# Optimization experiments

Measured on AMD Instinct MI355X. Metric: run time of the kernel, lower is better.

The kernel has to match this reference:

```python
import jax, jax.numpy as jnp
import numpy as np

B = 32            # graphs in batch
NPG = 2048        # nodes per graph (equal-size graphs -> static topk sizes)
N = B * NPG
DEG = 8
E = N * DEG
IN = 64
H1 = 2 * IN       # 128
H2 = 2 * H1       # 256
K1 = NPG // 2     # SAGPooling ratio=0.5
K2 = K1 // 2
EPS = 1e-5


def _lin(k, fi, fo):
    s = 1.0 / np.sqrt(fi)
    return jax.random.uniform(k, (fi, fo), jnp.float32, -s, s)


def setup_inputs() -> dict:
    key = jax.random.key(0)
    ks = jax.random.split(key, 24)
    x = jax.random.normal(ks[0], (N, IN), jnp.float32)
    # edges strictly within each graph
    eg = jnp.repeat(jnp.arange(B, dtype=jnp.int32), NPG * DEG)
    src = eg * NPG + jax.random.randint(ks[1], (E,), 0, NPG, jnp.int32)
    tgt = eg * NPG + jax.random.randint(ks[2], (E,), 0, NPG, jnp.int32)
    edge_index = jnp.stack([src, tgt])
    batch = jnp.repeat(jnp.arange(B, dtype=jnp.int32), NPG)
    return {
        "x": x, "edge_index": edge_index, "batch": batch,
        # SAGEConv1: lin_l (neighbors, with bias) + lin_r (root, no bias)
        "W1l": _lin(ks[3], IN, H1), "b1l": jnp.zeros((H1,), jnp.float32),
        "W1r": _lin(ks[4], IN, H1),
        "bn1_g": jnp.ones((H1,), jnp.float32), "bn1_b": jnp.zeros((H1,), jnp.float32),
        # SAGPooling1 scorer = GraphConv(H1, 1): lin_rel (sum-agg, bias) + lin_root
        "p1_Wrel": _lin(ks[5], H1, 1), "p1_brel": jnp.zeros((1,), jnp.float32),
        "p1_Wroot": _lin(ks[6], H1, 1),
        "W2l": _lin(ks[7], H1, H2), "b2l": jnp.zeros((H2,), jnp.float32),
        "W2r": _lin(ks[8], H1, H2),
        "bn2_g": jnp.ones((H2,), jnp.float32), "bn2_b": jnp.zeros((H2,), jnp.float32),
        "p2_Wrel": _lin(ks[9], H2, 1), "p2_brel": jnp.zeros((1,), jnp.float32),
        "p2_Wroot": _lin(ks[10], H2, 1),
        "Wlin": _lin(ks[11], H2, 2), "blin": jnp.zeros((2,), jnp.float32),
    }


def sage_conv(x, src, tgt, emask, Wl, bl, Wr, n):
    # PyG SAGEConv: mean-aggregate x_j over valid incoming edges, then lin_l(agg)+lin_r(x)
    msg = x[src] * emask[:, None]
    s = jax.ops.segment_sum(msg, tgt, num_segments=n)
    cnt = jax.ops.segment_sum(emask, tgt, num_segments=n)
    mean = s / jnp.maximum(cnt, 1.0)[:, None]
    return mean @ Wl + bl + x @ Wr


def graph_conv_score(x, src, tgt, emask, Wrel, brel, Wroot, n):
    # PyG GraphConv (sum aggregation), out_channels=1
    s = jax.ops.segment_sum(x[src] * emask[:, None], tgt, num_segments=n)
    return (s @ Wrel + brel + x @ Wroot)[:, 0]


def batch_norm(x, g, b):
    m = x.mean(0)
    v = jnp.mean((x - m) ** 2, 0)  # biased var, as BatchNorm1d training
    return (x - m) * jax.lax.rsqrt(v + EPS) * g + b


def sag_pool(x, src, tgt, emask, score, npg, k):
    # per-graph top-k by score; x_kept scaled by tanh(score); edges re-filtered via mask
    vals, idx = jax.lax.top_k(score.reshape(B, npg), k)          # [B,k]
    perm = (jnp.arange(B, dtype=jnp.int32)[:, None] * npg + idx.astype(jnp.int32)).reshape(-1)
    xnew = x[perm] * jnp.tanh(vals.reshape(-1))[:, None]
    mapping = jnp.full((x.shape[0],), -1, jnp.int32).at[perm].set(
        jnp.arange(B * k, dtype=jnp.int32))
    ns, nt = mapping[src], mapping[tgt]
    valid = emask * ((ns >= 0) & (nt >= 0)).astype(emask.dtype)
    return xnew, jnp.maximum(ns, 0), jnp.maximum(nt, 0), valid


def reference(x, edge_index, batch, W1l, b1l, W1r, bn1_g, bn1_b,
              p1_Wrel, p1_brel, p1_Wroot, W2l, b2l, W2r, bn2_g, bn2_b,
              p2_Wrel, p2_brel, p2_Wroot, Wlin, blin):
    src, tgt = edge_index[0], edge_index[1]
    emask = jnp.ones((src.shape[0],), x.dtype)

    h = sage_conv(x, src, tgt, emask, W1l, b1l, W1r, N)
    h = jax.nn.relu(batch_norm(h, bn1_g, bn1_b))
    s1 = graph_conv_score(h, src, tgt, emask, p1_Wrel, p1_brel, p1_Wroot, N)
    h, src, tgt, emask = sag_pool(h, src, tgt, emask, s1, NPG, K1)

    n1 = B * K1
    h = sage_conv(h, src, tgt, emask, W2l, b2l, W2r, n1)
    h = jax.nn.relu(batch_norm(h, bn2_g, bn2_b))
    s2 = graph_conv_score(h, src, tgt, emask, p2_Wrel, p2_brel, p2_Wroot, n1)
    h, src, tgt, emask = sag_pool(h, src, tgt, emask, s2, K1, K2)

    batch2 = jnp.repeat(jnp.arange(B, dtype=jnp.int32), K2)
    pooled = jax.ops.segment_sum(h, batch2, num_segments=B) / jnp.asarray(K2, h.dtype)
    out = jax.nn.relu(pooled) @ Wlin + blin
    return jax.nn.softmax(out, axis=1)
```

## Files before the change

### kernel.cpp

```cpp
#include <hip/hip_runtime.h>
#include <math.h>

#define Bg   32
#define NPGc 2048
#define Nn   (Bg*NPGc)
#define DEGc 8
#define Ee   (Nn*DEGc)
#define INc  64
#define H1c  128
#define H2c  256
#define K1c  1024
#define K2c  512
#define N1c  (Bg*K1c)
#define N2c  (Bg*K2c)
#define SLAB 64

typedef __attribute__((ext_vector_type(8))) short short8;
typedef __attribute__((ext_vector_type(4))) float f32x4;

__device__ __forceinline__ ushort f2bf(float f) {
    uint u = __float_as_uint(f);
    uint r = (u + 0x7fffu + ((u >> 16) & 1u)) >> 16;
    return (ushort)r;
}
__device__ __forceinline__ float bf2f(ushort v) { return __uint_as_float((uint)v << 16); }
__device__ __forceinline__ float bfhi(uint v) { return __uint_as_float(v & 0xffff0000u); }
__device__ __forceinline__ float bflo(uint v) { return __uint_as_float(v << 16); }
__device__ __forceinline__ uint fkey(float f) {
    uint u = __float_as_uint(f);
    return u ^ ((uint)((int)u >> 31) | 0x80000000u);
}
__device__ __forceinline__ void unpk8(uint4 v, float* f) {
    f[0] = bflo(v.x); f[1] = bfhi(v.x);
    f[2] = bflo(v.y); f[3] = bfhi(v.y);
    f[4] = bflo(v.z); f[5] = bfhi(v.z);
    f[6] = bflo(v.w); f[7] = bfhi(v.w);
}
__device__ __forceinline__ uint4 pack8(const float* a, float inv) {
    uint4 o;
    o.x = (uint)f2bf(a[0] * inv) | ((uint)f2bf(a[1] * inv) << 16);
    o.y = (uint)f2bf(a[2] * inv) | ((uint)f2bf(a[3] * inv) << 16);
    o.z = (uint)f2bf(a[4] * inv) | ((uint)f2bf(a[5] * inv) << 16);
    o.w = (uint)f2bf(a[6] * inv) | ((uint)f2bf(a[7] * inv) << 16);
    return o;
}
__device__ __forceinline__ void accf8(float* a, const float* p) {
    float4 u0 = *(const float4*)p;
    float4 u1 = *(const float4*)(p + 4);
    a[0] += u0.x; a[1] += u0.y; a[2] += u0.z; a[3] += u0.w;
    a[4] += u1.x; a[5] += u1.y; a[6] += u1.z; a[7] += u1.w;
}

__global__ void init_kernel(int4* __restrict__ wc1, int4* __restrict__ wc2,
                            int4* __restrict__ dstats) {
    int id = blockIdx.x * blockDim.x + threadIdx.x;
    int4 z = {0, 0, 0, 0};
    if (id < 16384) { wc1[id] = z; return; }
    id -= 16384;
    if (id < 8192)  { wc2[id] = z; return; }
    id -= 8192;
    if (id < 384)   { dstats[id] = z; }
}

__global__ void prep2_kernel(const int* __restrict__ src, const int* __restrict__ tgt,
                             const float* __restrict__ W1l, const float* __restrict__ W1r,
                             const float* __restrict__ W2l, const float* __restrict__ W2r,
                             ushort* __restrict__ T1l, ushort* __restrict__ T1r,
                             ushort* __restrict__ T2l, ushort* __restrict__ T2r,
                             int* __restrict__ wc1, int* __restrict__ col1) {
    int id = blockIdx.x * blockDim.x + threadIdx.x;
    if (id < Ee) {
        int t = tgt[id];
        int p = atomicAdd(&wc1[t], 1);
        col1[t * SLAB + p] = src[id];
        return;
    }
    id -= Ee;
    if (id < 8192) {
        int c = id / 64, k = id % 64;
        T1l[id] = f2bf(W1l[k * 128 + c]);
        T1r[id] = f2bf(W1r[k * 128 + c]);
        return;
    }
    id -= 8192;
    if (id < 32768) {
        int c = id / 128, k = id % 128;
        T2l[id] = f2bf(W2l[k * 256 + c]);
        T2r[id] = f2bf(W2r[k * 256 + c]);
    }
}
#define PREP2_TOTAL (Ee + 8192 + 32768)

__global__ __launch_bounds__(512) void gemm1f_kernel(
        const float* __restrict__ x, const int* __restrict__ deg,
        const int* __restrict__ col, const ushort* __restrict__ Wtl,
        const ushort* __restrict__ Wtr, const float* __restrict__ bias,
        ushort* __restrict__ out, double* __restrict__ dsum,
        double* __restrict__ dsq) {
    __shared__ ushort As[2][128][36];
    __shared__ ushort Bs[2][128][36];
    __shared__ float bsumS[2][128], bsqS[2][128];
    int b = blockIdx.x;
    int bs = ((b & 7) << 6) + (b >> 3);
    int m0 = bs << 7;
    int lane = threadIdx.x & 63;
    int wid = threadIdx.x >> 6;
    int wr = (wid & 1) << 6, wc = (wid >> 1) << 5;
    int l16 = lane & 15, quad = lane >> 4;

    int ar = threadIdx.x >> 2, ack = (threadIdx.x & 3) * 8;
    int anode = m0 + ar;
    int abg = anode * SLAB, adg = deg[anode];
    int4 c0h = *(const int4*)&col[abg];
    int4 c1h = *(const int4*)&col[abg + 4];
    int anb[8] = {c0h.x, c0h.y, c0h.z, c0h.w, c1h.x, c1h.y, c1h.z, c1h.w};

    f32x4 acc[4][2];
#pragma unroll
    for (int a = 0; a < 4; a++)
#pragma unroll
        for (int c = 0; c < 2; c++) acc[a][c] = (f32x4){0.f, 0.f, 0.f, 0.f};

    for (int kk0 = 0; kk0 < INc; kk0 += 32) {
        {
            int idx = threadIdx.x;
            int r = idx >> 2, ck = (idx & 3) * 8;
            *(uint4*)&Bs[0][r][ck] = *(const uint4*)&Wtl[(size_t)r * INc + kk0 + ck];
            *(uint4*)&Bs[1][r][ck] = *(const uint4*)&Wtr[(size_t)r * INc + kk0 + ck];
        }
        {
            const float* xp = &x[(size_t)anode * INc + kk0 + ack];
            float vals[8];
            float4 v0 = *(const float4*)xp, v1 = *(const float4*)(xp + 4);
            vals[0] = v0.x; vals[1] = v0.y; vals[2] = v0.z; vals[3] = v0.w;
            vals[4] = v1.x; vals[5] = v1.y; vals[6] = v1.z; vals[7] = v1.w;
            *(uint4*)&As[1][ar][ack] = pack8(vals, 1.f);
        }
        {
            float a[8] = {0.f, 0.f, 0.f, 0.f, 0.f, 0.f, 0.f, 0.f};
#pragma unroll
            for (int j = 0; j < 8; j++)
                if (j < adg) accf8(a, &x[(size_t)anb[j] * INc + kk0 + ack]);
            for (int i = abg + 8; i < abg + adg; i++)
                accf8(a, &x[(size_t)col[i] * INc + kk0 + ack]);
            int cdg = adg < 1 ? 1 : adg;
            *(uint4*)&As[0][ar][ack] = pack8(a, 1.f / (float)cdg);
        }
        __syncthreads();
        short8 a[2][4], bfr[2][2];
#pragma unroll
        for (int s = 0; s < 2; s++)
#pragma unroll
            for (int mt = 0; mt < 4; mt++)
                a[s][mt] = *(const short8*)&As[s][wr + mt * 16 + l16][quad * 8];
#pragma unroll
        for (int s = 0; s < 2; s++)
#pragma unroll
            for (int nt = 0; nt < 2; nt++)
                bfr[s][nt] = *(const short8*)&Bs[s][wc + nt * 16 + l16][quad * 8];
#pragma unroll
        for (int mt = 0; mt < 4; mt++)
#pragma unroll
            for (int nt = 0; nt < 2; nt++) {
                acc[mt][nt] = __builtin_amdgcn_mfma_f32_16x16x32_bf16(
                    a[0][mt], bfr[0][nt], acc[mt][nt], 0, 0, 0);
                acc[mt][nt] = __builtin_amdgcn_mfma_f32_16x16x32_bf16(
                    a[1][mt], bfr[1][nt], acc[mt][nt], 0, 0, 0);
            }
        __syncthreads();
    }
    float s[2] = {0.f, 0.f}, sq[2] = {0.f, 0.f};
#pragma unroll
    for (int nt = 0; nt < 2; nt++) {
        int colx = wc + nt * 16 + l16;
        float bv = bias[colx];
#pragma unroll
        for (int mt = 0; mt < 4; mt++)
#pragma unroll
            for (int rr = 0; rr < 4; rr++) {
                int row = m0 + wr + mt * 16 + quad * 4 + rr;
                float ov = acc[mt][nt][rr] + bv;
                out[(size_t)row * H1c + colx] = f2bf(ov);
                s[nt] += ov; sq[nt] += ov * ov;
            }
    }
#pragma unroll
    for (int nt = 0; nt < 2; nt++) {
        float ss = s[nt], qq = sq[nt];
        ss += __shfl_down(ss, 16); qq += __shfl_down(qq, 16);
        ss += __shfl_down(ss, 32); qq += __shfl_down(qq, 32);
        if (quad == 0) {
            bsumS[wid & 1][wc + nt * 16 + l16] = ss;
            bsqS[wid & 1][wc + nt * 16 + l16] = qq;
        }
    }
    __syncthreads();
    if (threadIdx.x < 128) {
        int c = threadIdx.x;
        atomicAdd(&dsum[c], (double)(bsumS[0][c] + bsumS[1][c]));
        atomicAdd(&dsq[c], (double)(bsqS[0][c] + bsqS[1][c]));
    }
}

template<int C>
__global__ __launch_bounds__(256) void score_kernel(const ushort* __restrict__ h,
                                                    const double* __restrict__ dsum,
                                                    const double* __restrict__ dsq,
                                                    const float* __restrict__ g,
                                                    const float* __restrict__ b,
                                                    const float* __restrict__ wrel,
                                                    const float* __restrict__ wroot,
                                                    float* __restrict__ r,
                                                    float* __restrict__ root, int n) {
    __shared__ float sc[C], sh[C], wrl[C], wrt[C];
    if ((int)threadIdx.x < C) {
        int c = threadIdx.x;
        double m = dsum[c] / (double)n;
        double var = dsq[c] / (double)n - m * m;
        float s = g[c] * (float)(1.0 / sqrt(var + 1e-5));
        sc[c] = s; sh[c] = b[c] - (float)m * s;
        wrl[c] = wrel[c]; wrt[c] = wroot[c];
    }
    __syncthreads();
    int gid = blockIdx.x * 256 + threadIdx.x;
    int node = gid >> 3, ln = gid & 7;
    float rr = 0.f, rt = 0.f;
#pragma unroll
    for (int p = 0; p < C / 64; p++) {
        int cb = p * 64 + ln * 8;
        uint4 v = *(const uint4*)&h[(size_t)node * C + cb];
        float vv[8];
        unpk8(v, vv);
#pragma unroll
        for (int q = 0; q < 8; q++) {
            int cc = cb + q;
            float val = fmaxf(vv[q] * sc[cc] + sh[cc], 0.f);
            rr += val * wrl[cc];
            rt += val * wrt[cc];
        }
    }
#pragma unroll
    for (int off = 4; off; off >>= 1) {
        rr += __shfl_down(rr, off);
        rt += __shfl_down(rt, off);
    }
    if (ln == 0) { r[node] = rr; root[node] = rt; }
}

__global__ void __launch_bounds__(1024) sel1_kernel(const float* __restrict__ r,
                                                    const float* __restrict__ root,
                                                    const int* __restrict__ deg,
                                                    const int* __restrict__ col,
                                                    const float* __restrict__ brel,
                                                    int* __restrict__ perm,
                                                    float* __restrict__ tval,
                                                    int* __restrict__ map) {
    __shared__ float rL[2048];
    __shared__ float svals[2048];
    __shared__ uint hist[257];
    __shared__ uint wsum[16];
    __shared__ uint s_b, s_rem;
    int g = blockIdx.x;
    int tid = threadIdx.x;
    int lane = tid & 63, wid = tid >> 6;
    int base = g * NPGc;
    rL[tid] = r[base + tid];
    rL[tid + 1024] = r[base + tid + 1024];
    if (tid < 257) hist[tid] = 0;
    __syncthreads();
    float bv = brel[0];
#pragma unroll
    for (int j = 0; j < 2; j++) {
        int i = tid + (j << 10);
        int node = base + i;
        float acc = bv + root[node];
        int e0 = node * SLAB, dg = deg[node];
        int4 c0 = *(const int4*)&col[e0];
        int4 c1 = *(const int4*)&col[e0 + 4];
        int nb[8] = {c0.x, c0.y, c0.z, c0.w, c1.x, c1.y, c1.z, c1.w};
#pragma unroll
        for (int q = 0; q < 8; q++)
            if (q < dg) acc += rL[nb[q] - base];
        for (int e = e0 + 8; e < e0 + dg; e++) acc += rL[col[e] - base];
        svals[i] = acc;
    }
    __syncthreads();

    uint prefix = 0, himask = 0, rem = (uint)K1c;
    for (int shift = 24; shift >= 0; shift -= 8) {
#pragma unroll
        for (int j = 0; j < 2; j++) {
            uint kk = fkey(svals[tid + (j << 10)]);
            if ((kk & himask) == prefix) atomicAdd(&hist[(kk >> shift) & 255], 1);
        }
        __syncthreads();
        if (tid < 64) {
            int L = tid;
            uint h0 = hist[4 * L], h1v = hist[4 * L + 1], h2v = hist[4 * L + 2],
                 h3 = hist[4 * L + 3];
            uint s3 = h3, s2 = h2v + s3, s1 = h1v + s2, s0 = h0 + s1;
            uint v = s0;
            for (int off = 1; off < 64; off <<= 1) {
                uint u = __shfl_down(v, off);
                if (L + off < 64) v += u;
            }
            uint above = v - s0;
            hist[4 * L] = s0 + above;
            hist[4 * L + 1] = s1 + above;
            hist[4 * L + 2] = s2 + above;
            hist[4 * L + 3] = s3 + above;
        }
        __syncthreads();
        if (tid < 256) {
            uint sb = hist[tid], sb1 = hist[tid + 1];
            if (sb >= rem && sb1 < rem) { s_b = (uint)tid; s_rem = rem - sb1; }
        }
        __syncthreads();
        prefix |= (s_b << shift);
        rem = s_rem;
        himask |= (0xFFu << shift);
        if (tid < 256) hist[tid] = 0;
        __syncthreads();
    }
    uint thr = prefix;
    uint tieM = rem;
    uint gcnt = 0, ecnt = 0, gflags = 0, eflags = 0;
#pragma unroll
    for (int j = 0; j < 2; j++) {
        uint kk = fkey(svals[tid + (j << 10)]);
        if (kk > thr) { gflags |= 1u << j; gcnt++; }
        else if (kk == thr) { eflags |= 1u << j; ecnt++; }
    }
    uint key = (gcnt << 16) | ecnt;
    uint v = key;
    for (int off = 1; off < 64; off <<= 1) {
        uint u = __shfl_up(v, off);
        if (lane >= off) v += u;
    }
    if (lane == 63) wsum[wid] = v;
    __syncthreads();
    if (tid < 16) {
        uint w0 = wsum[tid], w = w0;
        for (int off = 1; off < 16; off <<= 1) {
            uint u = __shfl_up(w, off);
            if ((int)tid >= off) w += u;
        }
        wsum[tid] = w - w0;
    }
    __syncthreads();
    uint excl = (v - key) + wsum[wid];
    uint gbase = excl >> 16, ebase = excl & 0xFFFFu;
#pragma unroll
    for (int j = 0; j < 2; j++) {
        bool gt = (gflags >> j) & 1u;
        bool eq = (eflags >> j) & 1u;
        int i = tid + (j << 10);
        int o = -1;
        if (gt || (eq && ebase < tieM)) {
            uint pos = gbase + min(ebase, tieM);
            o = g * K1c + (int)pos;
            perm[o] = base + i;
            tval[o] = tanhf(svals[i]);
        }
        map[base + i] = o;
        gbase += gt ? 1u : 0u;
        ebase += eq ? 1u : 0u;
    }
}

__global__ void fill2_kernel(const int* __restrict__ src, const int* __restrict__ tgt,
                             const int* __restrict__ map1,
                             int* __restrict__ wc2, int* __restrict__ col2) {
    int e = blockIdx.x * blockDim.x + threadIdx.x;
    if (e >= Ee) return;
    int nt = map1[tgt[e]];
    if (nt < 0) return;
    int ns = map1[src[e]];
    if (ns < 0) return;
    int p = atomicAdd(&wc2[nt], 1);
    col2[nt * SLAB + p] = ns;
}

__global__ __launch_bounds__(512) void gemm2f_kernel(
        const ushort* __restrict__ h1, const int* __restrict__ perm1,
        const float* __restrict__ tv1, const double* __restrict__ dsum1,
        const double* __restrict__ dsq1, const float* __restrict__ bn1g,
        const float* __restrict__ bn1b, const int* __restrict__ deg,
        const int* __restrict__ col, const ushort* __restrict__ Wtl,
        const ushort* __restrict__ Wtr, const float* __restrict__ bias,
        ushort* __restrict__ out, double* __restrict__ dsum,
        double* __restrict__ dsq) {
    __shared__ ushort As[2][128][36];
    __shared__ ushort Bs[2][256][36];
    __shared__ float bsumS[2][256], bsqS[2][256];
    __shared__ float sc1[128], sh1[128];
    int b = blockIdx.x;
    int bs = ((b & 7) << 5) + (b >> 3);
    int m0 = bs << 7;
    int lane = threadIdx.x & 63;
    int wid = threadIdx.x >> 6;
    int wr = (wid & 1) << 6, wc = (wid >> 1) << 6;
    int l16 = lane & 15, quad = lane >> 4;

    if (threadIdx.x < 128) {
        int c = threadIdx.x;
        double m = dsum1[c] / (double)Nn;
        double var = dsq1[c] / (double)Nn - m * m;
        float s = bn1g[c] * (float)(1.0 / sqrt(var + 1e-5));
        sc1[c] = s; sh1[c] = bn1b[c] - (float)m * s;
    }

    int ar = threadIdx.x >> 2, ack = (threadIdx.x & 3) * 8;
    int anode = m0 + ar;
    int aold = perm1[anode];
    float atv = tv1[anode];
    int abg = anode * SLAB, adg = deg[anode];
    int4 c0h = *(const int4*)&col[abg];
    int4 c1h = *(const int4*)&col[abg + 4];
    int anb[8] = {c0h.x, c0h.y, c0h.z, c0h.w, c1h.x, c1h.y, c1h.z, c1h.w};
    int aon[8]; float atn[8];
#pragma unroll
    for (int j = 0; j < 8; j++) {
        int nbv = (j < adg) ? anb[j] : anode;
        aon[j] = perm1[nbv];
        atn[j] = tv1[nbv];
    }
    __syncthreads();

    f32x4 acc[4][4];
#pragma unroll
    for (int a = 0; a < 4; a++)
#pragma unroll
        for (int c = 0; c < 4; c++) acc[a][c] = (f32x4){0.f, 0.f, 0.f, 0.f};

    for (int kk0 = 0; kk0 < H1c; kk0 += 32) {
        for (int idx = threadIdx.x; idx < 1024; idx += 512) {
            int r = idx >> 2, ck = (idx & 3) * 8;
            *(uint4*)&Bs[0][r][ck] = *(const uint4*)&Wtl[(size_t)r * H1c + kk0 + ck];
            *(uint4*)&Bs[1][r][ck] = *(const uint4*)&Wtr[(size_t)r * H1c + kk0 + ck];
        }
        {
            uint4 hv = *(const uint4*)&h1[((size_t)aold << 7) + kk0 + ack];
            float vals[8];
            unpk8(hv, vals);
#pragma unroll
            for (int q = 0; q < 8; q++) {
                int cc = kk0 + ack + q;
                vals[q] = fmaxf(vals[q] * sc1[cc] + sh1[cc], 0.f) * atv;
            }
            *(uint4*)&As[1][ar][ack] = pack8(vals, 1.f);
        }
        {
            float a[8] = {0.f, 0.f, 0.f, 0.f, 0.f, 0.f, 0.f, 0.f};
#pragma unroll
            for (int j = 0; j < 8; j++)
                if (j < adg) {
                    uint4 u = *(const uint4*)&h1[((size_t)aon[j] << 7) + kk0 + ack];
                    float f[8];
                    unpk8(u, f);
#pragma unroll
                    for (int q = 0; q < 8; q++) {
                        int cc = kk0 + ack + q;
                        a[q] += fmaxf(f[q] * sc1[cc] + sh1[cc], 0.f) * atn[j];
                    }
                }
            for (int i = abg + 8; i < abg + adg; i++) {
                int nbv = col[i];
                int on = perm1[nbv];
                float tn = tv1[nbv];
                uint4 u = *(const uint4*)&h1[((size_t)on << 7) + kk0 + ack];
                float f[8];
                unpk8(u, f);
#pragma unroll
                for (int q = 0; q < 8; q++) {
                    int cc = kk0 + ack + q;
                    a[q] += fmaxf(f[q] * sc1[cc] + sh1[cc], 0.f) * tn;
                }
            }
            int cdg = adg < 1 ? 1 : adg;
            *(uint4*)&As[0][ar][ack] = pack8(a, 1.f / (float)cdg);
        }
        __syncthreads();
        short8 a[2][4], bfr[2][4];
#pragma unroll
        for (int s = 0; s < 2; s++)
#pragma unroll
            for (int mt = 0; mt < 4; mt++)
                a[s][mt] = *(const short8*)&As[s][wr + mt * 16 + l16][quad * 8];
#pragma unroll
        for (int s = 0; s < 2; s++)
#pragma unroll
            for (int nt = 0; nt < 4; nt++)
                bfr[s][nt] = *(const short8*)&Bs[s][wc + nt * 16 + l16][quad * 8];
#pragma unroll
        for (int mt = 0; mt < 4; mt++)
#pragma unroll
            for (int nt = 0; nt < 4; nt++) {
                acc[mt][nt] = __builtin_amdgcn_mfma_f32_16x16x32_bf16(
                    a[0][mt], bfr[0][nt], acc[mt][nt], 0, 0, 0);
                acc[mt][nt] = __builtin_amdgcn_mfma_f32_16x16x32_bf16(
                    a[1][mt], bfr[1][nt], acc[mt][nt], 0, 0, 0);
            }
        __syncthreads();
    }
    float s[4] = {0.f, 0.f, 0.f, 0.f}, sq[4] = {0.f, 0.f, 0.f, 0.f};
#pragma unroll
    for (int nt = 0; nt < 4; nt++) {
        int colx = wc + nt * 16 + l16;
        float bv = bias[colx];
#pragma unroll
        for (int mt = 0; mt < 4; mt++)
#pragma unroll
            for (int rr = 0; rr < 4; rr++) {
                int row = m0 + wr + mt * 16 + quad * 4 + rr;
                float ov = acc[mt][nt][rr] + bv;
                out[(size_t)row * H2c + colx] = f2bf(ov);
                s[nt] += ov; sq[nt] += ov * ov;
            }
    }
#pragma unroll
    for (int nt = 0; nt < 4; nt++) {
        float ss = s[nt], qq = sq[nt];
        ss += __shfl_down(ss, 16); qq += __shfl_down(qq, 16);
        ss += __shfl_down(ss, 32); qq += __shfl_down(qq, 32);
        if (quad == 0) {
            bsumS[wid & 1][wc + nt * 16 + l16] = ss;
            bsqS[wid & 1][wc + nt * 16 + l16] = qq;
        }
    }
    __syncthreads();
    if (threadIdx.x < 256) {
        int c = threadIdx.x;
        atomicAdd(&dsum[c], (double)(bsumS[0][c] + bsumS[1][c]));
        atomicAdd(&dsq[c], (double)(bsqS[0][c] + bsqS[1][c]));
    }
}

__global__ void __launch_bounds__(1024) sel2pool_kernel(
        const float* __restrict__ r, const float* __restrict__ root,
        const int* __restrict__ deg, const int* __restrict__ col,
        const float* __restrict__ brel, const ushort* __restrict__ h2,
        const double* __restrict__ dsum, const double* __restrict__ dsq,
        const float* __restrict__ g_, const float* __restrict__ b_,
        const float* __restrict__ Wlin, const float* __restrict__ blin,
        float* __restrict__ out) {
    __shared__ float rL[1024];
    __shared__ float svals[1024];
    __shared__ uint hist[257];
    __shared__ uint wsum[16];
    __shared__ uint s_b, s_rem;
    __shared__ int permL[512];
    __shared__ float tvL[512];
    __shared__ float sc[256], sh[256];
    __shared__ float part2[32][256];
    int g = blockIdx.x;
    int tid = threadIdx.x;
    int lane = tid & 63, wid = tid >> 6;
    int base = g * K1c;
    if (tid < 256) {
        int c = tid;
        double m = dsum[c] / (double)N1c;
        double var = dsq[c] / (double)N1c - m * m;
        float s = g_[c] * (float)(1.0 / sqrt(var + 1e-5));
        sc[c] = s; sh[c] = b_[c] - (float)m * s;
    }
    rL[tid] = r[base + tid];
    if (tid < 257) hist[tid] = 0;
    __syncthreads();
    {
        int node = base + tid;
        float acc = brel[0] + root[node];
        int e0 = node * SLAB, dg = deg[node];
        int4 c0 = *(const int4*)&col[e0];
        int4 c1 = *(const int4*)&col[e0 + 4];
        int nb[8] = {c0.x, c0.y, c0.z, c0.w, c1.x, c1.y, c1.z, c1.w};
#pragma unroll
        for (int q = 0; q < 8; q++)
            if (q < dg) acc += rL[nb[q] - base];
        for (int e = e0 + 8; e < e0 + dg; e++) acc += rL[col[e] - base];
        svals[tid] = acc;
    }
    __syncthreads();

    uint prefix = 0, himask = 0, rem = (uint)K2c;
    for (int shift = 24; shift >= 0; shift -= 8) {
        {
            uint kk = fkey(svals[tid]);
            if ((kk & himask) == prefix) atomicAdd(&hist[(kk >> shift) & 255], 1);
        }
        __syncthreads();
        if (tid < 64) {
            int L = tid;
            uint h0 = hist[4 * L], h1v = hist[4 * L + 1], h2v = hist[4 * L + 2],
                 h3 = hist[4 * L + 3];
            uint s3 = h3, s2 = h2v + s3, s1 = h1v + s2, s0 = h0 + s1;
            uint v = s0;
            for (int off = 1; off < 64; off <<= 1) {
                uint u = __shfl_down(v, off);
                if (L + off < 64) v += u;
            }
            uint above = v - s0;
            hist[4 * L] = s0 + above;
            hist[4 * L + 1] = s1 + above;
            hist[4 * L + 2] = s2 + above;
            hist[4 * L + 3] = s3 + above;
        }
        __syncthreads();
        if (tid < 256) {
            uint sb = hist[tid], sb1 = hist[tid + 1];
            if (sb >= rem && sb1 < rem) { s_b = (uint)tid; s_rem = rem - sb1; }
        }
        __syncthreads();
        prefix |= (s_b << shift);
        rem = s_rem;
        himask |= (0xFFu << shift);
        if (tid < 256) hist[tid] = 0;
        __syncthreads();
    }
    uint thr = prefix;
    uint tieM = rem;

    uint kk = fkey(svals[tid]);
    bool gt = kk > thr, eq = kk == thr;
    uint key = (gt ? 0x10000u : 0u) | (eq ? 1u : 0u);
    uint v = key;
    for (int off = 1; off < 64; off <<= 1) {
        uint u = __shfl_up(v, off);
        if (lane >= off) v += u;
    }
    if (lane == 63) wsum[wid] = v;
    __syncthreads();
    if (tid < 16) {
        uint w0 = wsum[tid], w = w0;
        for (int off = 1; off < 16; off <<= 1) {
            uint u = __shfl_up(w, off);
            if ((int)tid >= off) w += u;
        }
        wsum[tid] = w - w0;
    }
    __syncthreads();
    uint excl = (v - key) + wsum[wid];
    uint gbase = excl >> 16, ebase = excl & 0xFFFFu;
    if (gt || (eq && ebase < tieM)) {
        uint pos = gbase + min(ebase, tieM);
        permL[pos] = base + tid;
        tvL[pos] = tanhf(svals[tid]);
    }
    __syncthreads();

    {
        int rl = tid & 31, rg = tid >> 5;
        float a[8] = {0.f, 0.f, 0.f, 0.f, 0.f, 0.f, 0.f, 0.f};
        for (int it = 0; it < 16; it++) {
            int j = rg + it * 32;
            int row = permL[j];
            float tv = tvL[j];
            uint4 hv = *(const uint4*)&h2[((size_t)row << 8) + rl * 8];
            float f[8];
            unpk8(hv, f);
#pragma unroll
            for (int q = 0; q < 8; q++) {
                int cc = rl * 8 + q;
                a[q] += fmaxf(f[q] * sc[cc] + sh[cc], 0.f) * tv;
            }
        }
#pragma unroll
        for (int q = 0; q < 8; q++) part2[rg][rl * 8 + q] = a[q];
    }
    __syncthreads();
    if (tid < 256) {
        float s = 0.f;
#pragma unroll
        for (int gg = 0; gg < 32; gg++) s += part2[gg][tid];
        float sv = fmaxf(s * (1.f / (float)K2c), 0.f);
        rL[tid] = sv * Wlin[tid * 2 + 0];
        rL[256 + tid] = sv * Wlin[tid * 2 + 1];
    }
    __syncthreads();
    for (int off = 128; off; off >>= 1) {
        if (tid < off) { rL[tid] += rL[tid + off]; rL[256 + tid] += rL[256 + tid + off]; }
        __syncthreads();
    }
    if (tid == 0) {
        float o0 = rL[0] + blin[0], o1 = rL[256] + blin[1];
        float m = fmaxf(o0, o1);
        float e0 = expf(o0 - m), e1 = expf(o1 - m);
        float inv = 1.f / (e0 + e1);
        out[g * 2 + 0] = e0 * inv;
        out[g * 2 + 1] = e1 * inv;
    }
}

extern "C" void kernel_launch(void* const* d_in, const int* in_sizes, int n_in,
                              void* d_out, int out_size, void* d_ws, size_t ws_size,
                              hipStream_t stream) {
    const float* x      = (const float*)d_in[0];
    const int*   ei     = (const int*)d_in[1];
    const int*   src    = ei;
    const int*   tgt    = ei + Ee;
    const float* W1l    = (const float*)d_in[3];
    const float* b1l    = (const float*)d_in[4];
    const float* W1r    = (const float*)d_in[5];
    const float* bn1g   = (const float*)d_in[6];
    const float* bn1b   = (const float*)d_in[7];
    const float* p1Wrel = (const float*)d_in[8];
    const float* p1brel = (const float*)d_in[9];
    const float* p1Wroot= (const float*)d_in[10];
    const float* W2l    = (const float*)d_in[11];
    const float* b2l    = (const float*)d_in[12];
    const float* W2r    = (const float*)d_in[13];
    const float* bn2g   = (const float*)d_in[14];
    const float* bn2b   = (const float*)d_in[15];
    const float* p2Wrel = (const float*)d_in[16];
    const float* p2brel = (const float*)d_in[17];
    const float* p2Wroot= (const float*)d_in[18];
    const float* Wlin   = (const float*)d_in[19];
    const float* blin   = (const float*)d_in[20];
    float* out = (float*)d_out;
    char* ws = (char*)d_ws;

    size_t o = 0;
    auto A = [&](size_t b) { size_t r = o; o += (b + 255) & ~(size_t)255; return r; };
    size_t oH1   = A((size_t)Nn * H1c * 2);
    size_t oH2   = A((size_t)N1c * H2c * 2);
    size_t oCol1 = A((size_t)Nn * SLAB * 4);
    size_t oCol2 = A((size_t)N1c * SLAB * 4);
    size_t oWc1  = A((size_t)Nn * 4);
    size_t oR1   = A((size_t)Nn * 4);
    size_t oRoot1= A((size_t)Nn * 4);
    size_t oMap1 = A((size_t)Nn * 4);
    size_t oPerm1= A((size_t)N1c * 4);
    size_t oTv1  = A((size_t)N1c * 4);
    size_t oWc2  = A((size_t)N1c * 4);
    size_t oR2   = A((size_t)N1c * 4);
    size_t oRoot2= A((size_t)N1c * 4);
    size_t oDst  = A(768 * 8);
    size_t oWt1l = A(8192 * 2);
    size_t oWt1r = A(8192 * 2);
    size_t oWt2l = A(32768 * 2);
    size_t oWt2r = A(32768 * 2);
    (void)ws_size; (void)in_sizes; (void)n_in; (void)out_size;

    ushort* h1   = (ushort*)(ws + oH1);
    ushort* h2   = (ushort*)(ws + oH2);
    int* col1    = (int*)(ws + oCol1);
    int* col2    = (int*)(ws + oCol2);
    int* wc1     = (int*)(ws + oWc1);
    float* r1    = (float*)(ws + oR1);
    float* root1 = (float*)(ws + oRoot1);
    int* map1    = (int*)(ws + oMap1);
    int* perm1   = (int*)(ws + oPerm1);
    float* tv1   = (float*)(ws + oTv1);
    int* wc2     = (int*)(ws + oWc2);
    float* r2    = (float*)(ws + oR2);
    float* root2 = (float*)(ws + oRoot2);
    double* dsum1= (double*)(ws + oDst);
    double* dsq1 = dsum1 + 128;
    double* dsum2= dsum1 + 256;
    double* dsq2 = dsum1 + 512;
    ushort* T1l  = (ushort*)(ws + oWt1l);
    ushort* T1r  = (ushort*)(ws + oWt1r);
    ushort* T2l  = (ushort*)(ws + oWt2l);
    ushort* T2r  = (ushort*)(ws + oWt2r);

    init_kernel<<<98, 256, 0, stream>>>((int4*)wc1, (int4*)wc2, (int4*)dsum1);

    prep2_kernel<<<PREP2_TOTAL / 256, 256, 0, stream>>>(
        src, tgt, W1l, W1r, W2l, W2r, T1l, T1r, T2l, T2r, wc1, col1);

    gemm1f_kernel<<<512, 512, 0, stream>>>(x, wc1, col1, T1l, T1r, b1l, h1,
                                           dsum1, dsq1);

    score_kernel<H1c><<<Nn / 32, 256, 0, stream>>>(h1, dsum1, dsq1, bn1g, bn1b, p1Wrel,
                                                   p1Wroot, r1, root1, Nn);

    sel1_kernel<<<Bg, 1024, 0, stream>>>(r1, root1, wc1, col1, p1brel, perm1, tv1, map1);

    fill2_kernel<<<Ee / 256, 256, 0, stream>>>(src, tgt, map1, wc2, col2);

    gemm2f_kernel<<<256, 512, 0, stream>>>(h1, perm1, tv1, dsum1, dsq1, bn1g, bn1b,
                                           wc2, col2, T2l, T2r, b2l, h2, dsum2, dsq2);

    score_kernel<H2c><<<N1c / 32, 256, 0, stream>>>(h2, dsum2, dsq2, bn2g, bn2b, p2Wrel,
                                                    p2Wroot, r2, root2, N1c);

    sel2pool_kernel<<<Bg, 1024, 0, stream>>>(r2, root2, wc2, col2, p2brel, h2, dsum2,
                                             dsq2, bn2g, bn2b, Wlin, blin, out);
}
```

Baseline: 222.6 us.

## Drop second-level adjacency build; reuse level-1 CSR via map; split final pooling

Removes the fill2 kernel that rebuilt a pooled-graph adjacency with atomics. gemm2f and sel2 now walk the original level-1 adjacency through the original node index (perm1) and filter neighbours with map1. The fused sel2pool kernel is split into a selection kernel that writes per-node tanh flags, a grid-parallel partial pooling kernel using atomics into a pooled buffer, and a small finalize kernel. This saves the edge pass and the col2 traffic, and spreads the final pooling over more blocks. The cost is extra map1 lookups per neighbour, scanning all K1 rows in pooling, and two more kernel launches.

```diff
diff --git a/kernel.cpp b/kernel.cpp
--- a/kernel.cpp
+++ b/kernel.cpp
@@ -51,16 +51,17 @@
     a[4] += u1.x; a[5] += u1.y; a[6] += u1.z; a[7] += u1.w;
 }
 
-__global__ void init_kernel(int4* __restrict__ wc1, int4* __restrict__ wc2,
-                            int4* __restrict__ dstats) {
+__global__ void init_kernel(int4* __restrict__ wc1, int4* __restrict__ dstats,
+                            int4* __restrict__ pooled) {
     int id = blockIdx.x * blockDim.x + threadIdx.x;
     int4 z = {0, 0, 0, 0};
     if (id < 16384) { wc1[id] = z; return; }
     id -= 16384;
-    if (id < 8192)  { wc2[id] = z; return; }
-    id -= 8192;
-    if (id < 384)   { dstats[id] = z; }
-}
+    if (id < 384)   { dstats[id] = z; return; }
+    id -= 384;
+    if (id < 2048)  { pooled[id] = z; }
+}
+#define INIT_TOTAL (16384 + 384 + 2048)
 
 __global__ void prep2_kernel(const int* __restrict__ src, const int* __restrict__ tgt,
                              const float* __restrict__ W1l, const float* __restrict__ W1r,
@@ -368,28 +369,15 @@
     }
 }
 
-__global__ void fill2_kernel(const int* __restrict__ src, const int* __restrict__ tgt,
-                             const int* __restrict__ map1,
-                             int* __restrict__ wc2, int* __restrict__ col2) {
-    int e = blockIdx.x * blockDim.x + threadIdx.x;
-    if (e >= Ee) return;
-    int nt = map1[tgt[e]];
-    if (nt < 0) return;
-    int ns = map1[src[e]];
-    if (ns < 0) return;
-    int p = atomicAdd(&wc2[nt], 1);
-    col2[nt * SLAB + p] = ns;
-}
-
 __global__ __launch_bounds__(512) void gemm2f_kernel(
         const ushort* __restrict__ h1, const int* __restrict__ perm1,
-        const float* __restrict__ tv1, const double* __restrict__ dsum1,
-        const double* __restrict__ dsq1, const float* __restrict__ bn1g,
-        const float* __restrict__ bn1b, const int* __restrict__ deg,
-        const int* __restrict__ col, const ushort* __restrict__ Wtl,
-        const ushort* __restrict__ Wtr, const float* __restrict__ bias,
-        ushort* __restrict__ out, double* __restrict__ dsum,
-        double* __restrict__ dsq) {
+        const float* __restrict__ tv1, const int* __restrict__ map1,
+        const double* __restrict__ dsum1, const double* __restrict__ dsq1,
+        const float* __restrict__ bn1g, const float* __restrict__ bn1b,
+        const int* __restrict__ deg1, const int* __restrict__ col1,
+        const ushort* __restrict__ Wtl, const ushort* __restrict__ Wtr,
+        const float* __restrict__ bias, ushort* __restrict__ out,
+        double* __restrict__ dsum, double* __restrict__ dsq) {
     __shared__ ushort As[2][128][36];
     __shared__ ushort Bs[2][256][36];
     __shared__ float bsumS[2][256], bsqS[2][256];
@@ -414,17 +402,26 @@
     int anode = m0 + ar;
     int aold = perm1[anode];
     float atv = tv1[anode];
-    int abg = anode * SLAB, adg = deg[anode];
-    int4 c0h = *(const int4*)&col[abg];
-    int4 c1h = *(const int4*)&col[abg + 4];
+    int abg = aold * SLAB, adg1 = deg1[aold];
+    int4 c0h = *(const int4*)&col1[abg];
+    int4 c1h = *(const int4*)&col1[abg + 4];
     int anb[8] = {c0h.x, c0h.y, c0h.z, c0h.w, c1h.x, c1h.y, c1h.z, c1h.w};
-    int aon[8]; float atn[8];
+    uint avmask = 0;
+    float atn[8];
+    int acnt = 0;
 #pragma unroll
     for (int j = 0; j < 8; j++) {
-        int nbv = (j < adg) ? anb[j] : anode;
-        aon[j] = perm1[nbv];
-        atn[j] = tv1[nbv];
-    }
+        bool inr = (j < adg1);
+        int s = inr ? anb[j] : aold;
+        anb[j] = s;
+        int m = map1[s];
+        bool valid = inr && (m >= 0);
+        avmask |= valid ? (1u << j) : 0u;
+        atn[j] = valid ? tv1[m] : 0.f;
+        acnt += valid ? 1 : 0;
+    }
+    for (int i = abg + 8; i < abg + adg1; i++)
+        if (map1[col1[i]] >= 0) acnt++;
     __syncthreads();
 
     f32x4 acc[4][4];
@@ -454,8 +451,8 @@
             float a[8] = {0.f, 0.f, 0.f, 0.f, 0.f, 0.f, 0.f, 0.f};
 #pragma unroll
             for (int j = 0; j < 8; j++)
-                if (j < adg) {
-                    uint4 u = *(const uint4*)&h1[((size_t)aon[j] << 7) + kk0 + ack];
+                if ((avmask >> j) & 1u) {
+                    uint4 u = *(const uint4*)&h1[((size_t)anb[j] << 7) + kk0 + ack];
                     float f[8];
                     unpk8(u, f);
 #pragma unroll
@@ -464,20 +461,22 @@
                         a[q] += fmaxf(f[q] * sc1[cc] + sh1[cc], 0.f) * atn[j];
                     }
                 }
-            for (int i = abg + 8; i < abg + adg; i++) {
-                int nbv = col[i];
-                int on = perm1[nbv];
-                float tn = tv1[nbv];
-                uint4 u = *(const uint4*)&h1[((size_t)on << 7) + kk0 + ack];
-                float f[8];
-                unpk8(u, f);
-#pragma unroll
-                for (int q = 0; q < 8; q++) {
-                    int cc = kk0 + ack + q;
-                    a[q] += fmaxf(f[q] * sc1[cc] + sh1[cc], 0.f) * tn;
+            for (int i = abg + 8; i < abg + adg1; i++) {
+                int s = col1[i];
+                int m = map1[s];
+                if (m >= 0) {
+                    float tn = tv1[m];
+                    uint4 u = *(const uint4*)&h1[((size_t)s << 7) + kk0 + ack];
+                    float f[8];
+                    unpk8(u, f);
+#pragma unroll
+                    for (int q = 0; q < 8; q++) {
+                        int cc = kk0 + ack + q;
+                        a[q] += fmaxf(f[q] * sc1[cc] + sh1[cc], 0.f) * tn;
+                    }
                 }
             }
-            int cdg = adg < 1 ? 1 : adg;
+            int cdg = acnt < 1 ? 1 : acnt;
             *(uint4*)&As[0][ar][ack] = pack8(a, 1.f / (float)cdg);
         }
         __syncthreads();
@@ -536,48 +535,41 @@
     }
 }
 
-__global__ void __launch_bounds__(1024) sel2pool_kernel(
+__global__ void __launch_bounds__(1024) sel2_kernel(
         const float* __restrict__ r, const float* __restrict__ root,
-        const int* __restrict__ deg, const int* __restrict__ col,
-        const float* __restrict__ brel, const ushort* __restrict__ h2,
-        const double* __restrict__ dsum, const double* __restrict__ dsq,
-        const float* __restrict__ g_, const float* __restrict__ b_,
-        const float* __restrict__ Wlin, const float* __restrict__ blin,
-        float* __restrict__ out) {
+        const int* __restrict__ perm1, const int* __restrict__ map1,
+        const int* __restrict__ deg1, const int* __restrict__ col1,
+        const float* __restrict__ brel, float* __restrict__ tvflag) {
     __shared__ float rL[1024];
     __shared__ float svals[1024];
     __shared__ uint hist[257];
     __shared__ uint wsum[16];
     __shared__ uint s_b, s_rem;
-    __shared__ int permL[512];
-    __shared__ float tvL[512];
-    __shared__ float sc[256], sh[256];
-    __shared__ float part2[32][256];
     int g = blockIdx.x;
     int tid = threadIdx.x;
     int lane = tid & 63, wid = tid >> 6;
     int base = g * K1c;
-    if (tid < 256) {
-        int c = tid;
-        double m = dsum[c] / (double)N1c;
-        double var = dsq[c] / (double)N1c - m * m;
-        float s = g_[c] * (float)(1.0 / sqrt(var + 1e-5));
-        sc[c] = s; sh[c] = b_[c] - (float)m * s;
-    }
     rL[tid] = r[base + tid];
     if (tid < 257) hist[tid] = 0;
     __syncthreads();
     {
         int node = base + tid;
+        int o = perm1[node];
         float acc = brel[0] + root[node];
-        int e0 = node * SLAB, dg = deg[node];
-        int4 c0 = *(const int4*)&col[e0];
-        int4 c1 = *(const int4*)&col[e0 + 4];
+        int e0 = o * SLAB, dg = deg1[o];
+        int4 c0 = *(const int4*)&col1[e0];
+        int4 c1 = *(const int4*)&col1[e0 + 4];
         int nb[8] = {c0.x, c0.y, c0.z, c0.w, c1.x, c1.y, c1.z, c1.w};
 #pragma unroll
         for (int q = 0; q < 8; q++)
-            if (q < dg) acc += rL[nb[q] - base];
-        for (int e = e0 + 8; e < e0 + dg; e++) acc += rL[col[e] - base];
+            if (q < dg) {
+                int m = map1[nb[q]];
+                if (m >= 0) acc += rL[m - base];
+            }
+        for (int e = e0 + 8; e < e0 + dg; e++) {
+            int m = map1[col1[e]];
+            if (m >= 0) acc += rL[m - base];
+        }
         svals[tid] = acc;
     }
     __syncthreads();
@@ -640,49 +632,54 @@
     }
     __syncthreads();
     uint excl = (v - key) + wsum[wid];
-    uint gbase = excl >> 16, ebase = excl & 0xFFFFu;
-    if (gt || (eq && ebase < tieM)) {
-        uint pos = gbase + min(ebase, tieM);
-        permL[pos] = base + tid;
-        tvL[pos] = tanhf(svals[tid]);
-    }
-    __syncthreads();
-
+    uint ebase = excl & 0xFFFFu;
+    bool selv = gt || (eq && ebase < tieM);
+    tvflag[base + tid] = selv ? tanhf(svals[tid]) : 0.f;
+}
+
+__global__ void __launch_bounds__(256) pool_part_kernel(
+        const ushort* __restrict__ h2, const float* __restrict__ tvflag,
+        const double* __restrict__ dsum, const double* __restrict__ dsq,
+        const float* __restrict__ g_, const float* __restrict__ b_,
+        float* __restrict__ pooled) {
+    __shared__ float sc[256], sh[256];
     {
-        int rl = tid & 31, rg = tid >> 5;
-        float a[8] = {0.f, 0.f, 0.f, 0.f, 0.f, 0.f, 0.f, 0.f};
-        for (int it = 0; it < 16; it++) {
-            int j = rg + it * 32;
-            int row = permL[j];
-            float tv = tvL[j];
-            uint4 hv = *(const uint4*)&h2[((size_t)row << 8) + rl * 8];
-            float f[8];
-            unpk8(hv, f);
-#pragma unroll
-            for (int q = 0; q < 8; q++) {
-                int cc = rl * 8 + q;
-                a[q] += fmaxf(f[q] * sc[cc] + sh[cc], 0.f) * tv;
-            }
-        }
-#pragma unroll
-        for (int q = 0; q < 8; q++) part2[rg][rl * 8 + q] = a[q];
-    }
-    __syncthreads();
-    if (tid < 256) {
-        float s = 0.f;
-#pragma unroll
-        for (int gg = 0; gg < 32; gg++) s += part2[gg][tid];
-        float sv = fmaxf(s * (1.f / (float)K2c), 0.f);
-        rL[tid] = sv * Wlin[tid * 2 + 0];
-        rL[256 + tid] = sv * Wlin[tid * 2 + 1];
-    }
+        int c = threadIdx.x;
+        double m = dsum[c] / (double)N1c;
+        double var = dsq[c] / (double)N1c - m * m;
+        float s = g_[c] * (float)(1.0 / sqrt(var + 1e-5));
+        sc[c] = s; sh[c] = b_[c] - (float)m * s;
+    }
+    __syncthreads();
+    int g = blockIdx.x, p = blockIdx.y, c = threadIdx.x;
+    float s = 0.f;
+    int n0 = g * K1c + p * 128;
+    for (int j = 0; j < 128; j++) {
+        float fl = tvflag[n0 + j];
+        if (fl != 0.f) {
+            float hv = bf2f(h2[((size_t)(n0 + j) << 8) + c]);
+            s += fmaxf(hv * sc[c] + sh[c], 0.f) * fl;
+        }
+    }
+    atomicAdd(&pooled[g * H2c + c], s);
+}
+
+__global__ void __launch_bounds__(256) pool_fin_kernel(const float* __restrict__ pooled,
+                                                       const float* __restrict__ Wlin,
+                                                       const float* __restrict__ blin,
+                                                       float* __restrict__ out) {
+    __shared__ float p0s[256], p1s[256];
+    int g = blockIdx.x, c = threadIdx.x;
+    float s = fmaxf(pooled[g * 256 + c] * (1.f / (float)K2c), 0.f);
+    p0s[c] = s * Wlin[c * 2 + 0];
+    p1s[c] = s * Wlin[c * 2 + 1];
     __syncthreads();
     for (int off = 128; off; off >>= 1) {
-        if (tid < off) { rL[tid] += rL[tid + off]; rL[256 + tid] += rL[256 + tid + off]; }
-        __syncthreads();
-    }
-    if (tid == 0) {
-        float o0 = rL[0] + blin[0], o1 = rL[256] + blin[1];
+        if (c < off) { p0s[c] += p0s[c + off]; p1s[c] += p1s[c + off]; }
+        __syncthreads();
+    }
+    if (c == 0) {
+        float o0 = p0s[0] + blin[0], o1 = p1s[0] + blin[1];
         float m = fmaxf(o0, o1);
         float e0 = expf(o0 - m), e1 = expf(o1 - m);
         float inv = 1.f / (e0 + e1);
@@ -724,36 +721,35 @@
     size_t oH1   = A((size_t)Nn * H1c * 2);
     size_t oH2   = A((size_t)N1c * H2c * 2);
     size_t oCol1 = A((size_t)Nn * SLAB * 4);
-    size_t oCol2 = A((size_t)N1c * SLAB * 4);
     size_t oWc1  = A((size_t)Nn * 4);
     size_t oR1   = A((size_t)Nn * 4);
     size_t oRoot1= A((size_t)Nn * 4);
     size_t oMap1 = A((size_t)Nn * 4);
     size_t oPerm1= A((size_t)N1c * 4);
     size_t oTv1  = A((size_t)N1c * 4);
-    size_t oWc2  = A((size_t)N1c * 4);
     size_t oR2   = A((size_t)N1c * 4);
     size_t oRoot2= A((size_t)N1c * 4);
+    size_t oFlag = A((size_t)N1c * 4);
     size_t oDst  = A(768 * 8);
     size_t oWt1l = A(8192 * 2);
     size_t oWt1r = A(8192 * 2);
     size_t oWt2l = A(32768 * 2);
     size_t oWt2r = A(32768 * 2);
+    size_t oPool = A(Bg * H2c * 4);
     (void)ws_size; (void)in_sizes; (void)n_in; (void)out_size;
 
     ushort* h1   = (ushort*)(ws + oH1);
     ushort* h2   = (ushort*)(ws + oH2);
     int* col1    = (int*)(ws + oCol1);
-    int* col2    = (int*)(ws + oCol2);
     int* wc1     = (int*)(ws + oWc1);
     float* r1    = (float*)(ws + oR1);
     float* root1 = (float*)(ws + oRoot1);
     int* map1    = (int*)(ws + oMap1);
     int* perm1   = (int*)(ws + oPerm1);
     float* tv1   = (float*)(ws + oTv1);
-    int* wc2     = (int*)(ws + oWc2);
     float* r2    = (float*)(ws + oR2);
     float* root2 = (float*)(ws + oRoot2);
+    float* tvflag= (float*)(ws + oFlag);
     double* dsum1= (double*)(ws + oDst);
     double* dsq1 = dsum1 + 128;
     double* dsum2= dsum1 + 256;
@@ -762,8 +758,10 @@
     ushort* T1r  = (ushort*)(ws + oWt1r);
     ushort* T2l  = (ushort*)(ws + oWt2l);
     ushort* T2r  = (ushort*)(ws + oWt2r);
-
-    init_kernel<<<98, 256, 0, stream>>>((int4*)wc1, (int4*)wc2, (int4*)dsum1);
+    float* pooled= (float*)(ws + oPool);
+
+    init_kernel<<<(INIT_TOTAL + 255) / 256, 256, 0, stream>>>(
+        (int4*)wc1, (int4*)dsum1, (int4*)pooled);
 
     prep2_kernel<<<PREP2_TOTAL / 256, 256, 0, stream>>>(
         src, tgt, W1l, W1r, W2l, W2r, T1l, T1r, T2l, T2r, wc1, col1);
@@ -776,14 +774,21 @@
 
     sel1_kernel<<<Bg, 1024, 0, stream>>>(r1, root1, wc1, col1, p1brel, perm1, tv1, map1);
 
-    fill2_kernel<<<Ee / 256, 256, 0, stream>>>(src, tgt, map1, wc2, col2);
-
-    gemm2f_kernel<<<256, 512, 0, stream>>>(h1, perm1, tv1, dsum1, dsq1, bn1g, bn1b,
-                                           wc2, col2, T2l, T2r, b2l, h2, dsum2, dsq2);
+    gemm2f_kernel<<<256, 512, 0, stream>>>(h1, perm1, tv1, map1, dsum1, dsq1, bn1g,
+                                           bn1b, wc1, col1, T2l, T2r, b2l, h2,
+                                           dsum2, dsq2);
 
     score_kernel<H2c><<<N1c / 32, 256, 0, stream>>>(h2, dsum2, dsq2, bn2g, bn2b, p2Wrel,
                                                     p2Wroot, r2, root2, N1c);
 
-    sel2pool_kernel<<<Bg, 1024, 0, stream>>>(r2, root2, wc2, col2, p2brel, h2, dsum2,
-                                             dsq2, bn2g, bn2b, Wlin, blin, out);
-}
+    sel2_kernel<<<Bg, 1024, 0, stream>>>(r2, root2, perm1, map1, wc1, col1, p2brel,
+                                         tvflag);
+
+    {
+        dim3 gp(Bg, K1c / 128);
+        pool_part_kernel<<<gp, 256, 0, stream>>>(h2, tvflag, dsum2, dsq2, bn2g, bn2b,
+                                                 pooled);
+    }
+
+    pool_fin_kernel<<<Bg, 256, 0, stream>>>(pooled, Wlin, blin, out);
+}
```

Measured after the change: 249.3 us. 1.12x slower.

## Build pooled adjacency by filtering level-1 CSR slabs per kept node

Applied to the files above, without the earlier changes.

Replaces the edge-parallel fill of the second-level adjacency, which scanned all edges and used atomics, with a node-parallel kernel. Each kept node reads its existing level-1 neighbor slab, remaps neighbors through map1 and writes the surviving ones plus the count directly. This removes the atomics, the per-edge traffic over the full edge list, and the zeroing of wc2 in init. Neighbor order within a slab is now deterministic, which may change floating-point summation order relative to the atomic version.

```diff
diff --git a/kernel.cpp b/kernel.cpp
--- a/kernel.cpp
+++ b/kernel.cpp
@@ -51,16 +51,14 @@
     a[4] += u1.x; a[5] += u1.y; a[6] += u1.z; a[7] += u1.w;
 }
 
-__global__ void init_kernel(int4* __restrict__ wc1, int4* __restrict__ wc2,
-                            int4* __restrict__ dstats) {
+__global__ void init_kernel(int4* __restrict__ wc1, int4* __restrict__ dstats) {
     int id = blockIdx.x * blockDim.x + threadIdx.x;
     int4 z = {0, 0, 0, 0};
     if (id < 16384) { wc1[id] = z; return; }
     id -= 16384;
-    if (id < 8192)  { wc2[id] = z; return; }
-    id -= 8192;
     if (id < 384)   { dstats[id] = z; }
 }
+#define INIT_TOTAL (16384 + 384)
 
 __global__ void prep2_kernel(const int* __restrict__ src, const int* __restrict__ tgt,
                              const float* __restrict__ W1l, const float* __restrict__ W1r,
@@ -368,17 +366,30 @@
     }
 }
 
-__global__ void fill2_kernel(const int* __restrict__ src, const int* __restrict__ tgt,
-                             const int* __restrict__ map1,
-                             int* __restrict__ wc2, int* __restrict__ col2) {
-    int e = blockIdx.x * blockDim.x + threadIdx.x;
-    if (e >= Ee) return;
-    int nt = map1[tgt[e]];
-    if (nt < 0) return;
-    int ns = map1[src[e]];
-    if (ns < 0) return;
-    int p = atomicAdd(&wc2[nt], 1);
-    col2[nt * SLAB + p] = ns;
+__global__ void __launch_bounds__(256) nofill2_kernel(
+        const int* __restrict__ perm1, const int* __restrict__ map1,
+        const int* __restrict__ deg1, const int* __restrict__ col1,
+        int* __restrict__ wc2, int* __restrict__ col2) {
+    int n = blockIdx.x * 256 + threadIdx.x;
+    int o = perm1[n];
+    int e0 = o * SLAB, dg = deg1[o];
+    int4 c0 = *(const int4*)&col1[e0];
+    int4 c1 = *(const int4*)&col1[e0 + 4];
+    int nb[8] = {c0.x, c0.y, c0.z, c0.w, c1.x, c1.y, c1.z, c1.w};
+    int cnt = 0;
+    int ob = n * SLAB;
+#pragma unroll
+    for (int j = 0; j < 8; j++) {
+        if (j < dg) {
+            int m = map1[nb[j]];
+            if (m >= 0) col2[ob + cnt++] = m;
+        }
+    }
+    for (int e = e0 + 8; e < e0 + dg; e++) {
+        int m = map1[col1[e]];
+        if (m >= 0) col2[ob + cnt++] = m;
+    }
+    wc2[n] = cnt;
 }
 
 __global__ __launch_bounds__(512) void gemm2f_kernel(
@@ -763,7 +774,8 @@
     ushort* T2l  = (ushort*)(ws + oWt2l);
     ushort* T2r  = (ushort*)(ws + oWt2r);
 
-    init_kernel<<<98, 256, 0, stream>>>((int4*)wc1, (int4*)wc2, (int4*)dsum1);
+    init_kernel<<<(INIT_TOTAL + 255) / 256, 256, 0, stream>>>(
+        (int4*)wc1, (int4*)dsum1);
 
     prep2_kernel<<<PREP2_TOTAL / 256, 256, 0, stream>>>(
         src, tgt, W1l, W1r, W2l, W2r, T1l, T1r, T2l, T2r, wc1, col1);
@@ -776,7 +788,7 @@
 
     sel1_kernel<<<Bg, 1024, 0, stream>>>(r1, root1, wc1, col1, p1brel, perm1, tv1, map1);
 
-    fill2_kernel<<<Ee / 256, 256, 0, stream>>>(src, tgt, map1, wc2, col2);
+    nofill2_kernel<<<N1c / 256, 256, 0, stream>>>(perm1, map1, wc1, col1, wc2, col2);
 
     gemm2f_kernel<<<256, 512, 0, stream>>>(h1, perm1, tv1, dsum1, dsq1, bn1g, bn1b,
                                            wc2, col2, T2l, T2r, b2l, h2, dsum2, dsq2);
```

Measured after the change: 220.5 us. Within noise of the previous version (-0.9%).
